# Kernel optimization log

Hardware: AMD Instinct MI355X
Metric: run time of the kernel (lower is better)

The kernel has to match this reference:

```python
import jax, jax.numpy as jnp
import numpy as np

B, T, D = 4, 2048, 1024
H = 16
DK = D // H
SCALE = 1.0 / np.sqrt(DK)
EPS_LN = 1e-5
EPS_NORM = 1e-8


def setup_inputs() -> dict:
    key = jax.random.key(0)
    ks = jax.random.split(key, 12)
    gain = 1.0 / np.sqrt(2.0)
    # xavier_uniform bound for square [D, D] weight with gain
    bound = gain * np.sqrt(6.0 / (D + D))

    def w(k):
        return jax.random.uniform(k, (D, D), jnp.float32, -bound, bound)

    return {
        "x": jax.random.normal(ks[0], (B, T, D), jnp.float32),
        "mask": jax.random.bernoulli(ks[1], 0.1, (B, T)),  # True = masked out
        "wq": w(ks[2]), "bq": jnp.zeros((D,), jnp.float32),
        "wk": w(ks[3]), "bk": jnp.zeros((D,), jnp.float32),
        "wv": w(ks[4]), "bv": jnp.zeros((D,), jnp.float32),
        "wo": w(ks[5]), "bo": jnp.zeros((D,), jnp.float32),
        "ln_g": jnp.ones((D,), jnp.float32),
        "ln_b": jnp.zeros((D,), jnp.float32),
    }


def _layernorm(x, g, b):
    mu = jnp.mean(x, axis=-1, keepdims=True)
    var = jnp.var(x, axis=-1, keepdims=True)
    return (x - mu) * jax.lax.rsqrt(var + EPS_LN) * g + b


def _l2norm(x):
    # torch F.normalize: x / clamp_min(||x||_2, eps)
    n = jnp.sqrt(jnp.sum(x * x, axis=-1, keepdims=True))
    return x / jnp.maximum(n, EPS_NORM)


def reference(x, mask, wq, bq, wk, bk, wv, bv, wo, bo, ln_g, ln_b):
    xn = _layernorm(x, ln_g, ln_b)  # q_norm applied to shared input

    def proj(w, bias):
        y = jnp.einsum("btd,ed->bte", xn, w) + bias
        return y.reshape(B, T, H, DK).transpose(0, 2, 1, 3)  # [B,H,T,DK]

    Q = _l2norm(proj(wq, bq))
    K = _l2norm(proj(wk, bk))
    V = proj(wv, bv)

    scores = jnp.einsum("bhqd,bhkd->bhqk", Q, K) * SCALE
    scores = jnp.clip(scores, -10.0, 10.0)
    scores = jnp.where(mask[:, None, None, :], -10000.0, scores)
    scores = scores - jnp.max(scores, axis=-1, keepdims=True)
    attn = jax.nn.softmax(scores, axis=-1)

    out = jnp.einsum("bhqk,bhkd->bhqd", attn, V)
    out = out.transpose(0, 2, 1, 3).reshape(B, T, D)
    out = jnp.einsum("btd,ed->bte", out, wo) + bo
    return out * 0.5
```

## Files before the change

### kernel.cpp

```cpp
#include <hip/hip_runtime.h>
#include <hip/hip_bf16.h>
#include <cstdint>
#include <cstddef>
#include <cstring>

typedef unsigned short u16;
typedef unsigned char u8;
typedef __attribute__((ext_vector_type(8))) short short8;
typedef __attribute__((ext_vector_type(4))) float f32x4;

#define B_    4
#define T_    2048
#define D_    1024
#define H_    16
#define DK_   64
#define QSCALE_ 0.18033688011112042f

__device__ __forceinline__ float bf2f(u16 u) {
    unsigned int x = ((unsigned int)u) << 16;
    float f; __builtin_memcpy(&f, &x, 4); return f;
}
__device__ __forceinline__ u16 f2bf(float f) {
    unsigned int x; __builtin_memcpy(&x, &f, 4);
    x += 0x7fffu + ((x >> 16) & 1u);
    return (u16)(x >> 16);
}

__global__ __launch_bounds__(256) void prep_kernel(
    const u16* __restrict__ x, const u8* __restrict__ m,
    const void* s0, const void* s1, const void* s2, const void* s3,
    const void* s4, const void* s5,
    u16* __restrict__ vecs, u8* __restrict__ nm, int* flag, int n)
{
    __shared__ int tot, sbits;
    int tid = threadIdx.x;
    if (tid == 0) { tot = 0; sbits = 0; }
    __syncthreads();
    int cnt = 0;
    for (int i = tid; i < 4096; i += 256) {
        int e = (x[2 * i] >> 7) & 0xFF;
        if (e > 137 || (e >= 1 && e < 97)) cnt++;
    }
    int bits = 0;
    for (int i = tid; i < n; i += 256)
        if (m[i]) bits |= (i & 7);
    for (int o = 1; o < 64; o <<= 1) { cnt += __shfl_xor(cnt, o); bits |= __shfl_xor(bits, o); }
    if ((tid & 63) == 0) { atomicAdd(&tot, cnt); if (bits) atomicOr(&sbits, bits); }
    __syncthreads();
    int f = (tot > 1024) ? 1 : 0;
    if (tid == 0) *flag = f;
    int b = sbits;
    int stride = (b & 1) ? 1 : (b & 2) ? 2 : (b & 4) ? 4 : 8;
    for (int i = tid; i < n; i += 256)
        nm[i] = m[(size_t)i * stride] ? 1 : 0;
    const void* ss[6] = {s0, s1, s2, s3, s4, s5};
    for (int t = 0; t < 6; t++) {
        const void* s = ss[t];
        for (int i = tid; i < 1024; i += 256)
            vecs[t * 1024 + i] = f ? f2bf(((const float*)s)[i]) : ((const u16*)s)[i];
    }
}

__global__ __launch_bounds__(256) void convert_w_kernel(
    const void* s0, const void* s1, const void* s2, const void* s3,
    u16* d0, u16* d1, u16* d2, u16* d3, const int* __restrict__ flag)
{
    const void* s; u16* d;
    if (blockIdx.y == 0)      { s = s0; d = d0; }
    else if (blockIdx.y == 1) { s = s1; d = d1; }
    else if (blockIdx.y == 2) { s = s2; d = d2; }
    else                      { s = s3; d = d3; }
    int i4 = blockIdx.x * 256 + threadIdx.x;
    if (*flag) {
        float4 v = ((const float4*)s)[i4];
        ushort4 o; o.x = f2bf(v.x); o.y = f2bf(v.y); o.z = f2bf(v.z); o.w = f2bf(v.w);
        ((ushort4*)d)[i4] = o;
    } else {
        ((ushort4*)d)[i4] = ((const ushort4*)s)[i4];
    }
}

__global__ __launch_bounds__(256) void ln_kernel(
    const void* __restrict__ x, const u16* __restrict__ g,
    const u16* __restrict__ be, u16* __restrict__ xn, const int* __restrict__ flag)
{
    int row = blockIdx.x;
    int t = threadIdx.x;
    float v[4];
    if (*flag) {
        float4 f4 = ((const float4*)x)[(size_t)row * 256 + t];
        v[0] = f4.x; v[1] = f4.y; v[2] = f4.z; v[3] = f4.w;
    } else {
        ushort4 uv = ((const ushort4*)x)[(size_t)row * 256 + t];
        v[0] = bf2f(uv.x); v[1] = bf2f(uv.y); v[2] = bf2f(uv.z); v[3] = bf2f(uv.w);
    }
    float s = v[0] + v[1] + v[2] + v[3];
    float q = v[0]*v[0] + v[1]*v[1] + v[2]*v[2] + v[3]*v[3];
    for (int o = 1; o < 64; o <<= 1) { s += __shfl_xor(s, o); q += __shfl_xor(q, o); }
    __shared__ float rs[4], rq[4];
    int wv = t >> 6, ln = t & 63;
    if (ln == 0) { rs[wv] = s; rq[wv] = q; }
    __syncthreads();
    s = rs[0] + rs[1] + rs[2] + rs[3];
    q = rq[0] + rq[1] + rq[2] + rq[3];
    float mu   = s * (1.0f / D_);
    float var  = q * (1.0f / D_) - mu * mu;
    float rstd = rsqrtf(var + 1e-5f);
    u16 o4[4];
    for (int i = 0; i < 4; i++) {
        float f = (v[i] - mu) * rstd * bf2f(g[t*4 + i]) + bf2f(be[t*4 + i]);
        o4[i] = f2bf(f);
    }
    ushort4 ov; ov.x = o4[0]; ov.y = o4[1]; ov.z = o4[2]; ov.w = o4[3];
    *(ushort4*)(xn + (size_t)row * D_ + t * 4) = ov;
}

__global__ __launch_bounds__(256) void gemm_bt(
    const u16* __restrict__ A,
    const u16* __restrict__ W0, const u16* __restrict__ W1, const u16* __restrict__ W2,
    const u16* __restrict__ bias_all, int bias_idx0,
    u16* __restrict__ C0, u16* __restrict__ C1, u16* __restrict__ C2,
    float scale, const int* __restrict__ flag, int use_flag, int qkv_mode)
{
    const int K = 1024, N = 1024;
    const u16* W; const u16* bias; u16* C;
    if (blockIdx.z == 0)      { W = W0; bias = bias_all + (size_t)bias_idx0 * 1024;       C = C0; }
    else if (blockIdx.z == 1) { W = W1; bias = bias_all + (size_t)(bias_idx0 + 1) * 1024; C = C1; }
    else                      { W = W2; bias = bias_all + (size_t)(bias_idx0 + 2) * 1024; C = C2; }

    __shared__ u16 As[128 * 32];
    __shared__ u16 Bs[128 * 32];

    int tid  = threadIdx.x;
    int wave = tid >> 6, lane = tid & 63;
    int wm = wave >> 1, wn = wave & 1;
    int quad = lane >> 4, l16 = lane & 15;
    int bm = blockIdx.y * 128, bn = blockIdx.x * 128;

    f32x4 acc[4][4];
    const f32x4 fz = {0.f, 0.f, 0.f, 0.f};
    for (int i = 0; i < 4; i++) for (int j = 0; j < 4; j++) acc[i][j] = fz;

    int srow = lane >> 2;
    int scol = (lane & 3) * 8;
    const u16* gA0 = A + (size_t)(bm + wave * 32 + srow) * K + scol;
    const u16* gB0 = W + (size_t)(bn + wave * 32 + srow) * K + scol;

    for (int k0 = 0; k0 < K; k0 += 32) {
        for (int i = 0; i < 2; i++) {
            __builtin_amdgcn_global_load_lds(
                (const __attribute__((address_space(1))) void*)(gA0 + (size_t)i * 16 * K + k0),
                (__attribute__((address_space(3))) void*)(As + (wave * 32 + i * 16) * 32),
                16, 0, 0);
            __builtin_amdgcn_global_load_lds(
                (const __attribute__((address_space(1))) void*)(gB0 + (size_t)i * 16 * K + k0),
                (__attribute__((address_space(3))) void*)(Bs + (wave * 32 + i * 16) * 32),
                16, 0, 0);
        }
        __syncthreads();
        short8 a[4], b[4];
        for (int i = 0; i < 4; i++)
            a[i] = *(const short8*)(As + (wm * 64 + i * 16 + l16) * 32 + quad * 8);
        for (int j = 0; j < 4; j++)
            b[j] = *(const short8*)(Bs + (wn * 64 + j * 16 + l16) * 32 + quad * 8);
        for (int i = 0; i < 4; i++)
            for (int j = 0; j < 4; j++)
                acc[i][j] = __builtin_amdgcn_mfma_f32_16x16x32_bf16(a[i], b[j], acc[i][j], 0, 0, 0);
        __syncthreads();
    }

    if (qkv_mode) {
        if (blockIdx.z == 2) {
            for (int j = 0; j < 4; j++) {
                int col = bn + wn * 64 + j * 16 + l16;
                int h = col >> 6, d = col & 63;
                float bi = bf2f(bias[col]);
                for (int i = 0; i < 4; i++) {
                    int row0 = bm + wm * 64 + i * 16 + quad * 4;
                    int bq = row0 >> 11, t0 = row0 & 2047;
                    ushort4 pk;
                    pk.x = f2bf(acc[i][j][0] + bi); pk.y = f2bf(acc[i][j][1] + bi);
                    pk.z = f2bf(acc[i][j][2] + bi); pk.w = f2bf(acc[i][j][3] + bi);
                    *(ushort4*)(C + ((size_t)((bq * 16 + h) * 64 + d)) * 2048 + t0) = pk;
                }
            }
        } else {
            float sc2 = (blockIdx.z == 0) ? QSCALE_ : 1.0f;
            float bi[4];
            for (int j = 0; j < 4; j++) bi[j] = bf2f(bias[bn + wn * 64 + j * 16 + l16]);
            for (int i = 0; i < 4; i++) {
                int row0 = bm + wm * 64 + i * 16 + quad * 4;
                for (int r = 0; r < 4; r++) {
                    float v[4]; float s = 0.f;
                    for (int j = 0; j < 4; j++) { v[j] = acc[i][j][r] + bi[j]; s += v[j] * v[j]; }
                    s += __shfl_xor(s, 1); s += __shfl_xor(s, 2);
                    s += __shfl_xor(s, 4); s += __shfl_xor(s, 8);
                    float scl = sc2 / fmaxf(sqrtf(s), 1e-8f);
                    for (int j = 0; j < 4; j++) {
                        int col = bn + wn * 64 + j * 16 + l16;
                        C[(size_t)(row0 + r) * N + col] = f2bf(v[j] * scl);
                    }
                }
            }
        }
        return;
    }

    int f32out = use_flag ? *flag : 0;
    for (int j = 0; j < 4; j++) {
        int col = bn + wn * 64 + j * 16 + l16;
        float bi = bf2f(bias[col]);
        for (int i = 0; i < 4; i++) {
            int row0 = bm + wm * 64 + i * 16 + quad * 4;
            for (int r = 0; r < 4; r++) {
                float o = (acc[i][j][r] + bi) * scale;
                if (f32out) ((float*)C)[(size_t)(row0 + r) * N + col] = o;
                else        C[(size_t)(row0 + r) * N + col] = f2bf(o);
            }
        }
    }
}

__global__ __launch_bounds__(256, 3) void attn_kernel(
    const u16* __restrict__ Q, const u16* __restrict__ Kg,
    const u16* __restrict__ Vt, const u8* __restrict__ nm,
    u16* __restrict__ Oout)
{
    __shared__ u16 Ks[64 * 72];
    __shared__ u16 VTs[64 * 72];
    __shared__ u16 Ps[128 * 72];
    __shared__ __align__(16) float msf[64];
    __shared__ float l_sh[128];

    int tid  = threadIdx.x;
    int wave = tid >> 6, lane = tid & 63;
    int quad = lane >> 4, l16 = lane & 15;
    int q0 = blockIdx.x * 128;
    int b  = blockIdx.y >> 4, h = blockIdx.y & 15;
    const size_t base  = (size_t)b * T_ * D_ + h * DK_;
    const size_t vbase = (size_t)((b * 16 + h) * 64) * T_;

    short8 qa[2][2];
    for (int g = 0; g < 2; g++) {
        const u16* qrow = Q + base + (size_t)(q0 + wave * 32 + g * 16 + l16) * D_;
        qa[g][0] = *(const short8*)(qrow + quad * 8);
        qa[g][1] = *(const short8*)(qrow + 32 + quad * 8);
    }

    int sr = tid >> 3;
    int sc = (tid & 7) * 8;
    const u8* mrow = nm + b * T_;

    for (int p = 0; p < 2; p++) {
        int r = sr + p * 32;
        *(short8*)(&Ks[r * 72 + sc])  = *(const short8*)(Kg + base + (size_t)r * D_ + sc);
        *(short8*)(&VTs[r * 72 + sc]) = *(const short8*)(Vt + vbase + (size_t)r * T_ + sc);
    }
    if (tid < 64) msf[tid] = mrow[tid] ? 0.f : 1.f;
    __syncthreads();

    const f32x4 fz = {0.f, 0.f, 0.f, 0.f};
    f32x4 o_acc[2][4];
    for (int g = 0; g < 2; g++) for (int j = 0; j < 4; j++) o_acc[g][j] = fz;
    float rowsum[2] = {0.f, 0.f};

    for (int kt = 0; kt < T_; kt += 64) {
        int ktn = (kt + 64) & (T_ - 1);
        short8 kpre[2], vpre[2];
        for (int p = 0; p < 2; p++) {
            int r = sr + p * 32;
            kpre[p] = *(const short8*)(Kg + base + (size_t)(ktn + r) * D_ + sc);
            vpre[p] = *(const short8*)(Vt + vbase + (size_t)r * T_ + ktn + sc);
        }
        u8 mpre = (tid < 64) ? mrow[ktn + tid] : (u8)0;

        for (int j = 0; j < 4; j++) {
            short8 kb0 = *(const short8*)(Ks + (j * 16 + l16) * 72 + quad * 8);
            short8 kb1 = *(const short8*)(Ks + (j * 16 + l16) * 72 + 32 + quad * 8);
            f32x4 pm4 = *(const f32x4*)&msf[j * 16 + quad * 4];
            for (int g = 0; g < 2; g++) {
                f32x4 s4 = __builtin_amdgcn_mfma_f32_16x16x32_bf16(kb0, qa[g][0], fz, 0, 0, 0);
                s4       = __builtin_amdgcn_mfma_f32_16x16x32_bf16(kb1, qa[g][1], s4, 0, 0, 0);
                float p0 = __builtin_exp2f(s4[0]) * pm4[0];
                float p1 = __builtin_exp2f(s4[1]) * pm4[1];
                float p2 = __builtin_exp2f(s4[2]) * pm4[2];
                float p3 = __builtin_exp2f(s4[3]) * pm4[3];
                rowsum[g] += (p0 + p1) + (p2 + p3);
                __hip_bfloat162 h01 = __float22bfloat162_rn(float2{p0, p1});
                __hip_bfloat162 h23 = __float22bfloat162_rn(float2{p2, p3});
                uint2 pk;
                __builtin_memcpy(&pk.x, &h01, 4);
                __builtin_memcpy(&pk.y, &h23, 4);
                *(uint2*)(Ps + (wave * 32 + g * 16 + l16) * 72 + j * 16 + quad * 4) = pk;
            }
        }

        short8 pa0[2], pa1[2];
        for (int g = 0; g < 2; g++) {
            pa0[g] = *(const short8*)(Ps + (wave * 32 + g * 16 + l16) * 72 + quad * 8);
            pa1[g] = *(const short8*)(Ps + (wave * 32 + g * 16 + l16) * 72 + 32 + quad * 8);
        }
        for (int j = 0; j < 4; j++) {
            short8 vb0 = *(const short8*)(VTs + (j * 16 + l16) * 72 + quad * 8);
            short8 vb1 = *(const short8*)(VTs + (j * 16 + l16) * 72 + 32 + quad * 8);
            for (int g = 0; g < 2; g++) {
                o_acc[g][j] = __builtin_amdgcn_mfma_f32_16x16x32_bf16(pa0[g], vb0, o_acc[g][j], 0, 0, 0);
                o_acc[g][j] = __builtin_amdgcn_mfma_f32_16x16x32_bf16(pa1[g], vb1, o_acc[g][j], 0, 0, 0);
            }
        }

        __syncthreads();
        for (int p = 0; p < 2; p++) {
            int r = sr + p * 32;
            *(short8*)(&Ks[r * 72 + sc])  = kpre[p];
            *(short8*)(&VTs[r * 72 + sc]) = vpre[p];
        }
        if (tid < 64) msf[tid] = mpre ? 0.f : 1.f;
        __syncthreads();
    }

    for (int g = 0; g < 2; g++) {
        float l = rowsum[g];
        l += __shfl_xor(l, 16);
        l += __shfl_xor(l, 32);
        if (quad == 0) l_sh[wave * 32 + g * 16 + l16] = l;
    }

    for (int g = 0; g < 2; g++) {
        for (int j = 0; j < 4; j++) {
            for (int r = 0; r < 4; r++) {
                int row = wave * 32 + g * 16 + quad * 4 + r;
                float ld = fmaxf(l_sh[row], 1e-20f);
                float o = o_acc[g][j][r] / ld;
                Oout[base + (size_t)(q0 + row) * D_ + j * 16 + l16] = f2bf(o);
            }
        }
    }
}

extern "C" void kernel_launch(void* const* d_in, const int* in_sizes, int n_in,
                              void* d_out, int out_size, void* d_ws, size_t ws_size,
                              hipStream_t stream)
{
    const void* x    = d_in[0];
    const u8*   mask = (const u8*)d_in[1];
    const void* wq   = d_in[2];
    const void* bq   = d_in[3];
    const void* wk   = d_in[4];
    const void* bk   = d_in[5];
    const void* wv   = d_in[6];
    const void* bv   = d_in[7];
    const void* wo   = d_in[8];
    const void* bo   = d_in[9];
    const void* lng  = d_in[10];
    const void* lnb  = d_in[11];

    const size_t NTOK = (size_t)B_ * T_;
    u16* xn  = (u16*)d_ws;
    u16* Kb  = xn + NTOK * D_;
    u16* Vtb = Kb + NTOK * D_;
    u16* wqc = Vtb + NTOK * D_;
    u16* wkc = wqc + (size_t)D_ * D_;
    u16* wvc = wkc + (size_t)D_ * D_;
    u16* woc = wvc + (size_t)D_ * D_;
    u16* vecs = woc + (size_t)D_ * D_;
    u8*  nm  = (u8*)(vecs + 6 * 1024);
    int* flag = (int*)(nm + 8192);
    u16* Qb  = (u16*)d_out;

    prep_kernel<<<dim3(1), 256, 0, stream>>>((const u16*)x, mask, bq, bk, bv, bo, lng, lnb,
                                             vecs, nm, flag, B_ * T_);
    convert_w_kernel<<<dim3(1024, 4), 256, 0, stream>>>(wq, wk, wv, wo, wqc, wkc, wvc, woc, flag);
    ln_kernel<<<dim3(NTOK), 256, 0, stream>>>(x, vecs + 4 * 1024, vecs + 5 * 1024, xn, flag);
    gemm_bt<<<dim3(8, 64, 3), 256, 0, stream>>>(xn, wqc, wkc, wvc, vecs, 0, Qb, Kb, Vtb, 1.0f, flag, 0, 1);
    attn_kernel<<<dim3(16, 64), 256, 0, stream>>>(Qb, Kb, Vtb, nm, xn);
    gemm_bt<<<dim3(8, 64, 1), 256, 0, stream>>>(xn, woc, woc, woc, vecs, 3, (u16*)d_out, (u16*)d_out, (u16*)d_out, 0.5f, flag, 1, 0);
}
```

Before: 381.6 us.

## Keep attention probabilities in registers and swizzle K/V shared memory

The P tile no longer round-trips through shared memory. The PV product now uses 16x16x16 MFMA with V as the A operand, so the S accumulator layout feeds directly as the B operand. K and V tiles get an XOR-swizzled unpadded shared layout, and the output store is vectorized using per-lane row sums, which drops the l_sh buffer. Together these cut LDS traffic and usage, and the occupancy hint is raised from 3 to 4 blocks, at the cost of twice as many smaller MFMAs for PV.

Result: slower. 405.2 us (+6.2%).

```diff
diff --git a/kernel.cpp b/kernel.cpp
--- a/kernel.cpp
+++ b/kernel.cpp
@@ -7,6 +7,7 @@
 typedef unsigned short u16;
 typedef unsigned char u8;
 typedef __attribute__((ext_vector_type(8))) short short8;
+typedef __attribute__((ext_vector_type(4))) short short4b;
 typedef __attribute__((ext_vector_type(4))) float f32x4;
 
 #define B_    4
@@ -221,16 +222,14 @@
     }
 }
 
-__global__ __launch_bounds__(256, 3) void attn_kernel(
+__global__ __launch_bounds__(256, 4) void attn_kernel(
     const u16* __restrict__ Q, const u16* __restrict__ Kg,
     const u16* __restrict__ Vt, const u8* __restrict__ nm,
     u16* __restrict__ Oout)
 {
-    __shared__ u16 Ks[64 * 72];
-    __shared__ u16 VTs[64 * 72];
-    __shared__ u16 Ps[128 * 72];
+    __shared__ __align__(16) u16 Ks[64 * 64];
+    __shared__ __align__(16) u16 VTs[64 * 64];
     __shared__ __align__(16) float msf[64];
-    __shared__ float l_sh[128];
 
     int tid  = threadIdx.x;
     int wave = tid >> 6, lane = tid & 63;
@@ -247,17 +246,31 @@
         qa[g][1] = *(const short8*)(qrow + 32 + quad * 8);
     }
 
-    int sr = tid >> 3;
-    int sc = (tid & 7) * 8;
+    int sr  = tid >> 3;
+    int sc8 = tid & 7;
     const u8* mrow = nm + b * T_;
+    int vj2 = sc8 >> 2, vjp = (sc8 >> 1) & 1, vq0 = (sc8 & 1) * 2;
 
     for (int p = 0; p < 2; p++) {
         int r = sr + p * 32;
-        *(short8*)(&Ks[r * 72 + sc])  = *(const short8*)(Kg + base + (size_t)r * D_ + sc);
-        *(short8*)(&VTs[r * 72 + sc]) = *(const short8*)(Vt + vbase + (size_t)r * T_ + sc);
+        short8 kv = *(const short8*)(Kg + base + (size_t)r * D_ + sc8 * 8);
+        *(short8*)(&Ks[r * 64 + ((sc8 ^ (r & 7)) * 8)]) = kv;
+        short8 vv = *(const short8*)(Vt + vbase + (size_t)r * T_ + sc8 * 8);
+        int c0 = (vj2 * 4 + vq0) ^ (r & 7);
+        int c1 = (vj2 * 4 + vq0 + 1) ^ (r & 7);
+        short4b vlo = {vv[0], vv[1], vv[2], vv[3]};
+        short4b vhi = {vv[4], vv[5], vv[6], vv[7]};
+        *(short4b*)(&VTs[r * 64 + c0 * 8 + vjp * 4]) = vlo;
+        *(short4b*)(&VTs[r * 64 + c1 * 8 + vjp * 4]) = vhi;
     }
     if (tid < 64) msf[tid] = mrow[tid] ? 0.f : 1.f;
     __syncthreads();
+
+    int kc = (quad ^ (l16 & 7)) * 8;
+    const u16* kb_lo = Ks  + l16 * 64 + kc;
+    const u16* kb_hi = Ks  + l16 * 64 + (kc ^ 32);
+    const u16* vb_lo = VTs + l16 * 64 + kc;
+    const u16* vb_hi = VTs + l16 * 64 + (kc ^ 32);
 
     const f32x4 fz = {0.f, 0.f, 0.f, 0.f};
     f32x4 o_acc[2][4];
@@ -269,51 +282,56 @@
         short8 kpre[2], vpre[2];
         for (int p = 0; p < 2; p++) {
             int r = sr + p * 32;
-            kpre[p] = *(const short8*)(Kg + base + (size_t)(ktn + r) * D_ + sc);
-            vpre[p] = *(const short8*)(Vt + vbase + (size_t)r * T_ + ktn + sc);
+            kpre[p] = *(const short8*)(Kg + base + (size_t)(ktn + r) * D_ + sc8 * 8);
+            vpre[p] = *(const short8*)(Vt + vbase + (size_t)r * T_ + ktn + sc8 * 8);
         }
         u8 mpre = (tid < 64) ? mrow[ktn + tid] : (u8)0;
 
-        for (int j = 0; j < 4; j++) {
-            short8 kb0 = *(const short8*)(Ks + (j * 16 + l16) * 72 + quad * 8);
-            short8 kb1 = *(const short8*)(Ks + (j * 16 + l16) * 72 + 32 + quad * 8);
-            f32x4 pm4 = *(const f32x4*)&msf[j * 16 + quad * 4];
-            for (int g = 0; g < 2; g++) {
-                f32x4 s4 = __builtin_amdgcn_mfma_f32_16x16x32_bf16(kb0, qa[g][0], fz, 0, 0, 0);
-                s4       = __builtin_amdgcn_mfma_f32_16x16x32_bf16(kb1, qa[g][1], s4, 0, 0, 0);
-                float p0 = __builtin_exp2f(s4[0]) * pm4[0];
-                float p1 = __builtin_exp2f(s4[1]) * pm4[1];
-                float p2 = __builtin_exp2f(s4[2]) * pm4[2];
-                float p3 = __builtin_exp2f(s4[3]) * pm4[3];
-                rowsum[g] += (p0 + p1) + (p2 + p3);
-                __hip_bfloat162 h01 = __float22bfloat162_rn(float2{p0, p1});
-                __hip_bfloat162 h23 = __float22bfloat162_rn(float2{p2, p3});
-                uint2 pk;
-                __builtin_memcpy(&pk.x, &h01, 4);
-                __builtin_memcpy(&pk.y, &h23, 4);
-                *(uint2*)(Ps + (wave * 32 + g * 16 + l16) * 72 + j * 16 + quad * 4) = pk;
-            }
-        }
-
-        short8 pa0[2], pa1[2];
-        for (int g = 0; g < 2; g++) {
-            pa0[g] = *(const short8*)(Ps + (wave * 32 + g * 16 + l16) * 72 + quad * 8);
-            pa1[g] = *(const short8*)(Ps + (wave * 32 + g * 16 + l16) * 72 + 32 + quad * 8);
-        }
-        for (int j = 0; j < 4; j++) {
-            short8 vb0 = *(const short8*)(VTs + (j * 16 + l16) * 72 + quad * 8);
-            short8 vb1 = *(const short8*)(VTs + (j * 16 + l16) * 72 + 32 + quad * 8);
-            for (int g = 0; g < 2; g++) {
-                o_acc[g][j] = __builtin_amdgcn_mfma_f32_16x16x32_bf16(pa0[g], vb0, o_acc[g][j], 0, 0, 0);
-                o_acc[g][j] = __builtin_amdgcn_mfma_f32_16x16x32_bf16(pa1[g], vb1, o_acc[g][j], 0, 0, 0);
+        for (int j2 = 0; j2 < 2; j2++) {
+            short4b pf[2][2];
+            for (int jp = 0; jp < 2; jp++) {
+                int j = j2 * 2 + jp;
+                short8 kb0 = *(const short8*)(kb_lo + j * 1024);
+                short8 kb1 = *(const short8*)(kb_hi + j * 1024);
+                f32x4 pm4 = *(const f32x4*)&msf[j * 16 + quad * 4];
+                for (int g = 0; g < 2; g++) {
+                    f32x4 s4 = __builtin_amdgcn_mfma_f32_16x16x32_bf16(kb0, qa[g][0], fz, 0, 0, 0);
+                    s4       = __builtin_amdgcn_mfma_f32_16x16x32_bf16(kb1, qa[g][1], s4, 0, 0, 0);
+                    float p0 = __builtin_exp2f(s4[0]) * pm4[0];
+                    float p1 = __builtin_exp2f(s4[1]) * pm4[1];
+                    float p2 = __builtin_exp2f(s4[2]) * pm4[2];
+                    float p3 = __builtin_exp2f(s4[3]) * pm4[3];
+                    rowsum[g] += (p0 + p1) + (p2 + p3);
+                    __hip_bfloat162 h01 = __float22bfloat162_rn(float2{p0, p1});
+                    __hip_bfloat162 h23 = __float22bfloat162_rn(float2{p2, p3});
+                    short4b pv;
+                    __builtin_memcpy(&pv, &h01, 4);
+                    __builtin_memcpy(((char*)&pv) + 4, &h23, 4);
+                    pf[g][jp] = pv;
+                }
+            }
+            const u16* vb = j2 ? vb_hi : vb_lo;
+            for (int jd = 0; jd < 4; jd++) {
+                short8 vv = *(const short8*)(vb + jd * 1024);
+                short4b va0 = {vv[0], vv[1], vv[2], vv[3]};
+                short4b va1 = {vv[4], vv[5], vv[6], vv[7]};
+                for (int g = 0; g < 2; g++) {
+                    o_acc[g][jd] = __builtin_amdgcn_mfma_f32_16x16x16bf16_1k(va0, pf[g][0], o_acc[g][jd], 0, 0, 0);
+                    o_acc[g][jd] = __builtin_amdgcn_mfma_f32_16x16x16bf16_1k(va1, pf[g][1], o_acc[g][jd], 0, 0, 0);
+                }
             }
         }
 
         __syncthreads();
         for (int p = 0; p < 2; p++) {
             int r = sr + p * 32;
-            *(short8*)(&Ks[r * 72 + sc])  = kpre[p];
-            *(short8*)(&VTs[r * 72 + sc]) = vpre[p];
+            *(short8*)(&Ks[r * 64 + ((sc8 ^ (r & 7)) * 8)]) = kpre[p];
+            int c0 = (vj2 * 4 + vq0) ^ (r & 7);
+            int c1 = (vj2 * 4 + vq0 + 1) ^ (r & 7);
+            short4b vlo = {vpre[p][0], vpre[p][1], vpre[p][2], vpre[p][3]};
+            short4b vhi = {vpre[p][4], vpre[p][5], vpre[p][6], vpre[p][7]};
+            *(short4b*)(&VTs[r * 64 + c0 * 8 + vjp * 4]) = vlo;
+            *(short4b*)(&VTs[r * 64 + c1 * 8 + vjp * 4]) = vhi;
         }
         if (tid < 64) msf[tid] = mpre ? 0.f : 1.f;
         __syncthreads();
@@ -323,17 +341,15 @@
         float l = rowsum[g];
         l += __shfl_xor(l, 16);
         l += __shfl_xor(l, 32);
-        if (quad == 0) l_sh[wave * 32 + g * 16 + l16] = l;
-    }
-
-    for (int g = 0; g < 2; g++) {
-        for (int j = 0; j < 4; j++) {
-            for (int r = 0; r < 4; r++) {
-                int row = wave * 32 + g * 16 + quad * 4 + r;
-                float ld = fmaxf(l_sh[row], 1e-20f);
-                float o = o_acc[g][j][r] / ld;
-                Oout[base + (size_t)(q0 + row) * D_ + j * 16 + l16] = f2bf(o);
-            }
+        float inv = 1.0f / fmaxf(l, 1e-20f);
+        size_t orow = base + (size_t)(q0 + wave * 32 + g * 16 + l16) * D_;
+        for (int jd = 0; jd < 4; jd++) {
+            ushort4 pk;
+            pk.x = f2bf(o_acc[g][jd][0] * inv);
+            pk.y = f2bf(o_acc[g][jd][1] * inv);
+            pk.z = f2bf(o_acc[g][jd][2] * inv);
+            pk.w = f2bf(o_acc[g][jd][3] * inv);
+            *(ushort4*)(Oout + orow + jd * 16 + quad * 4) = pk;
         }
     }
 }
```
